# Optimization experiments

Measured on AMD Instinct MI355X. Metric: run time of the kernel, lower is better.

## Reference

```python
import jax, jax.numpy as jnp
import numpy as np

B, C, H, W = 8, 32, 256, 448


def setup_inputs() -> dict:
    key = jax.random.key(0)
    k1, k2 = jax.random.split(key)
    input1 = jax.random.normal(k1, (B, C, H, W), dtype=jnp.float32)
    input2 = jax.random.normal(k2, (B, 2, H, W), dtype=jnp.float32)  # flow (u, v)
    return {"input1": input1, "input2": input2, "kernel_size": 1}


def _forward_splat(input1, input2):
    """Forward warp: splat each source pixel to (x+u, y+v) with bilinear weights,
    accumulating via scatter-add (kernel_size=1 -> 2x2 bilinear footprint)."""
    b, c, h, w = input1.shape
    u = input2[:, 0]  # [B,H,W] horizontal flow
    v = input2[:, 1]  # [B,H,W] vertical flow
    xs = jnp.arange(w, dtype=input2.dtype)
    ys = jnp.arange(h, dtype=input2.dtype)
    tx = xs[None, None, :] + u  # target x, [B,H,W]
    ty = ys[None, :, None] + v  # target y, [B,H,W]
    x0 = jnp.floor(tx).astype(jnp.int32)
    y0 = jnp.floor(ty).astype(jnp.int32)
    fx = tx - x0.astype(tx.dtype)
    fy = ty - y0.astype(ty.dtype)

    vals = input1.transpose(0, 2, 3, 1).reshape(b * h * w, c)  # [BHW, C]
    out = jnp.zeros((b * h * w, c), dtype=input1.dtype)
    batch_off = (jnp.arange(b, dtype=jnp.int32) * (h * w))[:, None, None]

    for dx, dy in ((0, 0), (1, 0), (0, 1), (1, 1)):
        xx = x0 + dx
        yy = y0 + dy
        wx = fx if dx == 1 else (1.0 - fx)
        wy = fy if dy == 1 else (1.0 - fy)
        wgt = wx * wy  # [B,H,W]
        valid = (xx >= 0) & (xx < w) & (yy >= 0) & (yy < h)
        wgt = jnp.where(valid, wgt, 0.0)
        idx = batch_off + jnp.clip(yy, 0, h - 1) * w + jnp.clip(xx, 0, w - 1)
        out = out.at[idx.reshape(-1)].add(wgt.reshape(-1, 1) * vals)

    return out.reshape(b, h, w, c).transpose(0, 3, 1, 2)


def reference(input1, input2, kernel_size):
    # kernel_size=1 corresponds to the standard bilinear (2x2) splat footprint.
    return _forward_splat(input1, input2)
```

## Files before the change

### kernel.cpp

```cpp
#include <hip/hip_runtime.h>

constexpr int B = 8;
constexpr int C = 32;
constexpr int H = 256;
constexpr int W = 448;
constexpr int HW = H * W;

constexpr int TW  = 32;
constexpr int TH  = 16;
constexpr int RAD = 3;
constexpr int WX  = TW + 2 * RAD;
constexpr int WY  = TH + 2 * RAD;
constexpr int NSRC = WX * WY;
constexpr int NT  = 512;
constexpr int SITER = (NSRC + NT - 1) / NT;

__global__ __launch_bounds__(NT)
void splat_out(const float* __restrict__ in1,
               const float* __restrict__ flow,
               float* __restrict__ out,
               unsigned* __restrict__ wcnt,
               unsigned* __restrict__ wlist,
               unsigned cap) {
    __shared__ unsigned geomR[NSRC];
    __shared__ unsigned geomW2[2 * NSRC];
    __shared__ float4   valA[NSRC];
    __shared__ float4   valB[NSRC];

    int bid = blockIdx.x;
    int b = bid & 7;
    int t = bid >> 3;
    int ty = t / 14;
    int tx = t - ty * 14;
    int ox = tx * TW, oy = ty * TH;
    int tid = threadIdx.x;
    int qlx = tid & 31, qly = tid >> 5;
    int qx = ox + qlx, qy = oy + qly;

    int sg[SITER];
    const int fbase = b * 2 * HW;
#pragma unroll
    for (int j = 0; j < SITER; ++j) {
        int i = tid + j * NT;
        if (i < NSRC) {
            int wy = i / WX, wx = i - wy * WX;
            int sx = ox + wx - RAD, sy = oy + wy - RAD;
            int cx = min(max(sx, 0), W - 1), cy = min(max(sy, 0), H - 1);
            int g = cy * W + cx;
            sg[j] = g;
            unsigned gr = 0xFFu, wlo = 0u, whi = 0u;
            if (sx == cx && sy == cy) {
                float u = flow[fbase + g];
                float v = flow[fbase + g + HW];
                float txf = (float)sx + u;
                float tyf = (float)sy + v;
                float x0f = floorf(txf), y0f = floorf(tyf);
                int rx = (int)x0f - sx, ry = (int)y0f - sy;
                if (rx >= -RAD && rx <= RAD - 1 && ry >= -RAD && ry <= RAD - 1) {
                    float fx = txf - x0f, fy = tyf - y0f;
                    unsigned q00 = __float2uint_rn((1.f - fx) * (1.f - fy) * 65535.f);
                    unsigned q10 = __float2uint_rn(fx * (1.f - fy) * 65535.f);
                    unsigned q01 = __float2uint_rn((1.f - fx) * fy * 65535.f);
                    unsigned q11 = __float2uint_rn(fx * fy * 65535.f);
                    wlo = q00 | (q10 << 16);
                    whi = q01 | (q11 << 16);
                    gr = (unsigned)(rx + RAD) | ((unsigned)(ry + RAD) << 3);
                } else if (wx >= RAD && wx < RAD + TW && wy >= RAD && wy < RAD + TH) {
                    unsigned slot = atomicAdd(wcnt, 1u);
                    if (slot < cap) wlist[slot] = ((unsigned)b << 17) | (unsigned)g;
                }
            }
            geomR[i] = gr;
            geomW2[2 * i]     = wlo;
            geomW2[2 * i + 1] = whi;
        }
    }
    __syncthreads();

    unsigned long long mAll = 0ull, mDx = 0ull, mDy = 0ull;
    const int qbase = (qly + RAD) * WX + (qlx + RAD);
#pragma unroll
    for (int dy = -RAD; dy <= RAD; ++dy) {
#pragma unroll
        for (int dx = -RAD; dx <= RAD; ++dx) {
            unsigned g = geomR[qbase + dy * WX + dx];
            int tX = (int)(g & 7u) + dx;
            int tY = (int)((g >> 3) & 0x1Fu) + dy;
            bool mx = (unsigned)(tX - 2) <= 1u;
            bool my = (unsigned)(tY - 2) <= 1u;
            constexpr_unused:;
            const int j = (dy + RAD) * 8 + (dx + RAD);
            unsigned long long bit = (mx && my) ? (1ull << j) : 0ull;
            mAll |= bit;
            if (!(tX & 1)) mDx |= bit;
            if (!(tY & 1)) mDy |= bit;
        }
    }

    const float* inb  = in1 + (size_t)b * C * HW;
    float*       outb = out + (size_t)b * C * HW;
    int qg = qy * W + qx;
    const int joff = 3 * WX + 3;

    for (int c = 0; c < C; c += 8) {
        const float* p = inb + (size_t)c * HW;
        __syncthreads();
#pragma unroll
        for (int j = 0; j < SITER; ++j) {
            int i = tid + j * NT;
            if (i < NSRC) {
                int g = sg[j];
                valA[i] = make_float4(p[g], p[g + HW], p[g + 2 * HW], p[g + 3 * HW]);
                const float* p4 = p + 4 * HW;
                valB[i] = make_float4(p4[g], p4[g + HW], p4[g + 2 * HW], p4[g + 3 * HW]);
            }
        }
        __syncthreads();

        float a0 = 0.f, a1 = 0.f, a2 = 0.f, a3 = 0.f;
        float a4 = 0.f, a5 = 0.f, a6 = 0.f, a7 = 0.f;
        unsigned long long m = mAll;
        while (m) {
            int j = (int)__builtin_ctzll(m);
            m &= m - 1;
            int wi = qbase + ((j >> 3) * WX + (j & 7)) - joff;
            unsigned dyy = (unsigned)(mDy >> j) & 1u;
            unsigned dxx = (unsigned)(mDx >> j) & 1u;
            unsigned wd = geomW2[2 * wi + dyy];
            float w = (float)((wd >> (16u * dxx)) & 0xFFFFu) * (1.0f / 65535.0f);
            float4 vA = valA[wi];
            float4 vB = valB[wi];
            a0 = fmaf(w, vA.x, a0); a1 = fmaf(w, vA.y, a1);
            a2 = fmaf(w, vA.z, a2); a3 = fmaf(w, vA.w, a3);
            a4 = fmaf(w, vB.x, a4); a5 = fmaf(w, vB.y, a5);
            a6 = fmaf(w, vB.z, a6); a7 = fmaf(w, vB.w, a7);
        }
        float* o = outb + (size_t)c * HW + qg;
        o[0]      = a0; o[HW]     = a1; o[2 * HW] = a2; o[3 * HW] = a3;
        o[4 * HW] = a4; o[5 * HW] = a5; o[6 * HW] = a6; o[7 * HW] = a7;
    }
}

__global__ void outlier_list(const float* __restrict__ in1,
                             const float* __restrict__ flow,
                             float* __restrict__ out,
                             const unsigned* __restrict__ wcnt,
                             const unsigned* __restrict__ wlist,
                             unsigned cap) {
    unsigned n = *wcnt;
    if (n > cap) return;
    unsigned total = n * 8u;
    for (unsigned idx = blockIdx.x * blockDim.x + threadIdx.x;
         idx < total; idx += gridDim.x * blockDim.x) {
        unsigned e = wlist[idx >> 3];
        int c0 = (int)(idx & 7u) * 4;
        int bb = (int)(e >> 17);
        int p  = (int)(e & 0x1FFFFu);
        int y = p / W, x = p - y * W;

        float u = flow[(bb * 2 + 0) * HW + p];
        float v = flow[(bb * 2 + 1) * HW + p];
        float txf = (float)x + u;
        float tyf = (float)y + v;
        float fx0 = floorf(txf), fy0 = floorf(tyf);
        int x0 = (int)fx0, y0 = (int)fy0;
        float fx = txf - fx0, fy = tyf - fy0;
        float w00 = (1.0f - fx) * (1.0f - fy);
        float w10 = fx * (1.0f - fy);
        float w01 = (1.0f - fx) * fy;
        float w11 = fx * fy;
        bool vx0 = (x0 >= 0) && (x0 < W);
        bool vx1 = (x0 + 1 >= 0) && (x0 + 1 < W);
        bool vy0 = (y0 >= 0) && (y0 < H);
        bool vy1 = (y0 + 1 >= 0) && (y0 + 1 < H);
        long o00 = (long)y0 * W + x0;

        const float* src  = in1 + (size_t)bb * C * HW + (size_t)c0 * HW + p;
        float*       dstb = out + (size_t)bb * C * HW + (size_t)c0 * HW;
        for (int c = 0; c < 4; ++c) {
            float val = src[(size_t)c * HW];
            float* ob = dstb + (size_t)c * HW;
            if (vx0 && vy0) atomicAdd(ob + o00,         w00 * val);
            if (vx1 && vy0) atomicAdd(ob + o00 + 1,     w10 * val);
            if (vx0 && vy1) atomicAdd(ob + o00 + W,     w01 * val);
            if (vx1 && vy1) atomicAdd(ob + o00 + W + 1, w11 * val);
        }
    }
}

__global__ void outlier_fallback(const float* __restrict__ in1,
                                 const float* __restrict__ flow,
                                 float* __restrict__ out,
                                 const unsigned* __restrict__ wcnt,
                                 unsigned cap) {
    if (*wcnt <= cap) return;
    int npix = B * HW;
    for (int idx = blockIdx.x * blockDim.x + threadIdx.x;
         idx < npix; idx += gridDim.x * blockDim.x) {
        int b = idx / HW;
        int p = idx - b * HW;
        int y = p / W, x = p - y * W;
        float u = flow[(b * 2 + 0) * HW + p];
        float v = flow[(b * 2 + 1) * HW + p];
        float txf = (float)x + u;
        float tyf = (float)y + v;
        float fx0 = floorf(txf), fy0 = floorf(tyf);
        int x0 = (int)fx0, y0 = (int)fy0;
        int rx = x0 - x, ry = y0 - y;
        bool handled = (rx >= -RAD) && (rx <= RAD - 1) &&
                       (ry >= -RAD) && (ry <= RAD - 1);
        if (handled) continue;
        float fx = txf - fx0, fy = tyf - fy0;
        float w00 = (1.0f - fx) * (1.0f - fy);
        float w10 = fx * (1.0f - fy);
        float w01 = (1.0f - fx) * fy;
        float w11 = fx * fy;
        bool vx0 = (x0 >= 0) && (x0 < W);
        bool vx1 = (x0 + 1 >= 0) && (x0 + 1 < W);
        bool vy0 = (y0 >= 0) && (y0 < H);
        bool vy1 = (y0 + 1 >= 0) && (y0 + 1 < H);
        long o00 = (long)y0 * W + x0;
        const float* src = in1 + (size_t)b * C * HW + p;
        float* dstb = out + (size_t)b * C * HW;
        for (int c = 0; c < C; ++c) {
            float val = src[(size_t)c * HW];
            float* ob = dstb + (size_t)c * HW;
            if (vx0 && vy0) atomicAdd(ob + o00,         w00 * val);
            if (vx1 && vy0) atomicAdd(ob + o00 + 1,     w10 * val);
            if (vx0 && vy1) atomicAdd(ob + o00 + W,     w01 * val);
            if (vx1 && vy1) atomicAdd(ob + o00 + W + 1, w11 * val);
        }
    }
}

extern "C" void kernel_launch(void* const* d_in, const int* in_sizes, int n_in,
                              void* d_out, int out_size, void* d_ws, size_t ws_size,
                              hipStream_t stream) {
    const float* in1  = (const float*)d_in[0];
    const float* flow = (const float*)d_in[1];
    float* out = (float*)d_out;

    unsigned* wcnt  = (unsigned*)d_ws;
    unsigned* wlist = wcnt + 4;
    unsigned cap = 0;
    if (ws_size >= 64) {
        size_t c = ws_size / sizeof(unsigned) - 4;
        cap = (c > 0x7FFFFFFFull) ? 0x7FFFFFFFu : (unsigned)c;
    }

    hipMemsetAsync(wcnt, 0, sizeof(unsigned), stream);

    int nblocks = B * (H / TH) * (W / TW);
    splat_out<<<nblocks, NT, 0, stream>>>(in1, flow, out, wcnt, wlist, cap);

    outlier_list<<<256, 256, 0, stream>>>(in1, flow, out, wcnt, wlist, cap);
    outlier_fallback<<<256, 256, 0, stream>>>(in1, flow, out, wcnt, cap);
}
```

Baseline: 129.8 us.

## Stage all channels in LDS as fp16 and accumulate with packed half FMA

Converts source values and bilinear weights to packed fp16, stages all 32 channels of the halo window in shared memory at once, and accumulates with packed half2 FMAs in a single gather pass. This removes the four channel-group passes with their per-pass barriers and repeated mask walks, and halves LDS value traffic. The cost is reduced precision: fp16 storage of inputs and fp16 accumulation with round-toward-zero conversion may exceed tolerance. The larger LDS footprint may also lower occupancy.

```diff
diff --git a/kernel.cpp b/kernel.cpp
--- a/kernel.cpp
+++ b/kernel.cpp
@@ -1,4 +1,5 @@
 #include <hip/hip_runtime.h>
+#include <hip/hip_fp16.h>
 
 constexpr int B = 8;
 constexpr int C = 32;
@@ -15,6 +16,16 @@
 constexpr int NT  = 512;
 constexpr int SITER = (NSRC + NT - 1) / NT;
 
+static __device__ __forceinline__ unsigned pkrtz(float a, float b) {
+    return __builtin_bit_cast(unsigned, __builtin_amdgcn_cvt_pkrtz(a, b));
+}
+
+static __device__ __forceinline__ __half2 h2(unsigned u) {
+    union { unsigned u; __half2 h; } x;
+    x.u = u;
+    return x.h;
+}
+
 __global__ __launch_bounds__(NT)
 void splat_out(const float* __restrict__ in1,
                const float* __restrict__ flow,
@@ -23,9 +34,8 @@
                unsigned* __restrict__ wlist,
                unsigned cap) {
     __shared__ unsigned geomR[NSRC];
-    __shared__ unsigned geomW2[2 * NSRC];
-    __shared__ float4   valA[NSRC];
-    __shared__ float4   valB[NSRC];
+    __shared__ unsigned geomW[2 * NSRC];
+    __shared__ uint4    valV[4 * NSRC];
 
     int bid = blockIdx.x;
     int b = bid & 7;
@@ -58,12 +68,8 @@
                 int rx = (int)x0f - sx, ry = (int)y0f - sy;
                 if (rx >= -RAD && rx <= RAD - 1 && ry >= -RAD && ry <= RAD - 1) {
                     float fx = txf - x0f, fy = tyf - y0f;
-                    unsigned q00 = __float2uint_rn((1.f - fx) * (1.f - fy) * 65535.f);
-                    unsigned q10 = __float2uint_rn(fx * (1.f - fy) * 65535.f);
-                    unsigned q01 = __float2uint_rn((1.f - fx) * fy * 65535.f);
-                    unsigned q11 = __float2uint_rn(fx * fy * 65535.f);
-                    wlo = q00 | (q10 << 16);
-                    whi = q01 | (q11 << 16);
+                    wlo = pkrtz((1.f - fx) * (1.f - fy), fx * (1.f - fy));
+                    whi = pkrtz((1.f - fx) * fy,         fx * fy);
                     gr = (unsigned)(rx + RAD) | ((unsigned)(ry + RAD) << 3);
                 } else if (wx >= RAD && wx < RAD + TW && wy >= RAD && wy < RAD + TH) {
                     unsigned slot = atomicAdd(wcnt, 1u);
@@ -71,11 +77,30 @@
                 }
             }
             geomR[i] = gr;
-            geomW2[2 * i]     = wlo;
-            geomW2[2 * i + 1] = whi;
+            geomW[2 * i]     = wlo;
+            geomW[2 * i + 1] = whi;
         }
     }
     __syncthreads();
+
+    const float* inb = in1 + (size_t)b * C * HW;
+#pragma unroll
+    for (int j = 0; j < SITER; ++j) {
+        int i = tid + j * NT;
+        if (i < NSRC) {
+            const float* p = inb + sg[j];
+#pragma unroll
+            for (int q = 0; q < 4; ++q) {
+                const float* pq = p + (size_t)(8 * q) * HW;
+                uint4 vq;
+                vq.x = pkrtz(pq[0],              pq[(size_t)HW]);
+                vq.y = pkrtz(pq[(size_t)2 * HW], pq[(size_t)3 * HW]);
+                vq.z = pkrtz(pq[(size_t)4 * HW], pq[(size_t)5 * HW]);
+                vq.w = pkrtz(pq[(size_t)6 * HW], pq[(size_t)7 * HW]);
+                valV[4 * i + q] = vq;
+            }
+        }
+    }
 
     unsigned long long mAll = 0ull, mDx = 0ull, mDy = 0ull;
     const int qbase = (qly + RAD) * WX + (qlx + RAD);
@@ -88,7 +113,6 @@
             int tY = (int)((g >> 3) & 0x1Fu) + dy;
             bool mx = (unsigned)(tX - 2) <= 1u;
             bool my = (unsigned)(tY - 2) <= 1u;
-            constexpr_unused:;
             const int j = (dy + RAD) * 8 + (dx + RAD);
             unsigned long long bit = (mx && my) ? (1ull << j) : 0ull;
             mAll |= bit;
@@ -96,48 +120,40 @@
             if (!(tY & 1)) mDy |= bit;
         }
     }
-
-    const float* inb  = in1 + (size_t)b * C * HW;
-    float*       outb = out + (size_t)b * C * HW;
-    int qg = qy * W + qx;
+    __syncthreads();
+
+    __half2 acc2[16];
+#pragma unroll
+    for (int k = 0; k < 16; ++k) acc2[k] = h2(0u);
+
     const int joff = 3 * WX + 3;
-
-    for (int c = 0; c < C; c += 8) {
-        const float* p = inb + (size_t)c * HW;
-        __syncthreads();
-#pragma unroll
-        for (int j = 0; j < SITER; ++j) {
-            int i = tid + j * NT;
-            if (i < NSRC) {
-                int g = sg[j];
-                valA[i] = make_float4(p[g], p[g + HW], p[g + 2 * HW], p[g + 3 * HW]);
-                const float* p4 = p + 4 * HW;
-                valB[i] = make_float4(p4[g], p4[g + HW], p4[g + 2 * HW], p4[g + 3 * HW]);
-            }
-        }
-        __syncthreads();
-
-        float a0 = 0.f, a1 = 0.f, a2 = 0.f, a3 = 0.f;
-        float a4 = 0.f, a5 = 0.f, a6 = 0.f, a7 = 0.f;
-        unsigned long long m = mAll;
-        while (m) {
-            int j = (int)__builtin_ctzll(m);
-            m &= m - 1;
-            int wi = qbase + ((j >> 3) * WX + (j & 7)) - joff;
-            unsigned dyy = (unsigned)(mDy >> j) & 1u;
-            unsigned dxx = (unsigned)(mDx >> j) & 1u;
-            unsigned wd = geomW2[2 * wi + dyy];
-            float w = (float)((wd >> (16u * dxx)) & 0xFFFFu) * (1.0f / 65535.0f);
-            float4 vA = valA[wi];
-            float4 vB = valB[wi];
-            a0 = fmaf(w, vA.x, a0); a1 = fmaf(w, vA.y, a1);
-            a2 = fmaf(w, vA.z, a2); a3 = fmaf(w, vA.w, a3);
-            a4 = fmaf(w, vB.x, a4); a5 = fmaf(w, vB.y, a5);
-            a6 = fmaf(w, vB.z, a6); a7 = fmaf(w, vB.w, a7);
-        }
-        float* o = outb + (size_t)c * HW + qg;
-        o[0]      = a0; o[HW]     = a1; o[2 * HW] = a2; o[3 * HW] = a3;
-        o[4 * HW] = a4; o[5 * HW] = a5; o[6 * HW] = a6; o[7 * HW] = a7;
+    unsigned long long m = mAll;
+    while (m) {
+        int j = (int)__builtin_ctzll(m);
+        m &= m - 1;
+        int wi = qbase + ((j >> 3) * WX + (j & 7)) - joff;
+        unsigned dyy = (unsigned)(mDy >> j) & 1u;
+        unsigned dxx = (unsigned)(mDx >> j) & 1u;
+        unsigned wd = geomW[2 * wi + dyy];
+        unsigned hw = (wd >> (16u * dxx)) & 0xFFFFu;
+        __half2 w2 = h2(hw | (hw << 16));
+#pragma unroll
+        for (int q = 0; q < 4; ++q) {
+            uint4 v = valV[4 * wi + q];
+            acc2[4 * q + 0] = __hfma2(h2(v.x), w2, acc2[4 * q + 0]);
+            acc2[4 * q + 1] = __hfma2(h2(v.y), w2, acc2[4 * q + 1]);
+            acc2[4 * q + 2] = __hfma2(h2(v.z), w2, acc2[4 * q + 2]);
+            acc2[4 * q + 3] = __hfma2(h2(v.w), w2, acc2[4 * q + 3]);
+        }
+    }
+
+    float* o = out + (size_t)b * C * HW + qy * W + qx;
+#pragma unroll
+    for (int k = 0; k < 16; ++k) {
+        int c0 = 8 * (k >> 2) + 2 * (k & 3);
+        float2 f = __half22float2(acc2[k]);
+        o[(size_t)c0 * HW]       = f.x;
+        o[(size_t)(c0 + 1) * HW] = f.y;
     }
 }
 
```

New measurement: 124.0 us. 4.4% less time.
